# Kernel optimization log

Hardware: AMD Instinct MI355X
Metric: run time of the kernel (lower is better)

## Reference

```python
import jax, jax.numpy as jnp
import numpy as np

N = 50000          # nodes
E = 800000         # directed edges (before self loops)
H = 2              # attention heads
NEG_SLOPE = 0.2    # PyG GATv2 default
EPS = 1e-5         # GraphNorm eps
DIMS = [(3, 64), (64, 64), (64, 64)]


def _gatv2_layer(x, Wl, Wr, att, b, src, dst):
    # x: [N, din]; Wl, Wr: [din, H*C]; att: [H, C]; b: [C]
    n = x.shape[0]
    h, c = att.shape
    xl = (x @ Wl).reshape(n, h, c)   # source-side transform
    xr = (x @ Wr).reshape(n, h, c)   # target-side transform
    # edge-wise GATv2 score: a . leaky_relu(xl[j] + xr[i])
    e = jax.nn.leaky_relu(xl[src] + xr[dst], NEG_SLOPE)      # [E, H, C]
    logit = jnp.einsum('ehc,hc->eh', e, att)                 # [E, H]
    # segment softmax over incoming edges of each target node
    m = jax.ops.segment_max(logit, dst, num_segments=n)      # [N, H]
    a = jnp.exp(logit - m[dst])
    z = jax.ops.segment_sum(a, dst, num_segments=n)
    alpha = a / z[dst]                                       # [E, H]
    out = jax.ops.segment_sum(alpha[:, :, None] * xl[src], dst, num_segments=n)  # [N, H, C]
    return out.mean(axis=1) + b                              # concat=False -> head mean


def _graph_norm(x, w, b, ms):
    # single-graph GraphNorm: x -> w * (x - ms*mean) / sqrt(var + eps) + b
    mu = x.mean(axis=0)
    o = x - ms * mu
    var = (o * o).mean(axis=0)
    return w * o * jax.lax.rsqrt(var + EPS) + b


def setup_inputs() -> dict:
    key = jax.random.key(0)
    ks = jax.random.split(key, 2 + 3 * len(DIMS))
    inp = {
        'x': jax.random.normal(ks[0], (N, 3), dtype=jnp.float32),
        'edge_index': jax.random.randint(ks[1], (2, E), 0, N, dtype=jnp.int32),
    }
    for i, (din, dout) in enumerate(DIMS, start=1):
        k0, k1, k2 = ks[2 + 3 * (i - 1):2 + 3 * i]
        s_in = np.float32(1.0 / np.sqrt(din))
        s_att = np.float32(1.0 / np.sqrt(dout))
        inp[f'Wl{i}'] = jax.random.normal(k0, (din, H * dout), dtype=jnp.float32) * s_in
        inp[f'Wr{i}'] = jax.random.normal(k1, (din, H * dout), dtype=jnp.float32) * s_in
        inp[f'att{i}'] = jax.random.normal(k2, (H, dout), dtype=jnp.float32) * s_att
        inp[f'b{i}'] = jnp.zeros((dout,), dtype=jnp.float32)
        inp[f'gw{i}'] = jnp.ones((dout,), dtype=jnp.float32)
        inp[f'gb{i}'] = jnp.zeros((dout,), dtype=jnp.float32)
        inp[f'gm{i}'] = jnp.ones((dout,), dtype=jnp.float32)
    return inp


def reference(x, edge_index,
              Wl1, Wr1, att1, b1, gw1, gb1, gm1,
              Wl2, Wr2, att2, b2, gw2, gb2, gm2,
              Wl3, Wr3, att3, b3, gw3, gb3, gm3):
    n = x.shape[0]
    loop = jnp.arange(n, dtype=edge_index.dtype)
    src = jnp.concatenate([edge_index[0], loop])  # add_self_loops=True
    dst = jnp.concatenate([edge_index[1], loop])
    layers = [(Wl1, Wr1, att1, b1, gw1, gb1, gm1),
              (Wl2, Wr2, att2, b2, gw2, gb2, gm2),
              (Wl3, Wr3, att3, b3, gw3, gb3, gm3)]
    for Wl, Wr, att, b, gw, gb, gm in layers:
        x = _gatv2_layer(x, Wl, Wr, att, b, src, dst)
        x = jax.nn.relu(_graph_norm(x, gw, gb, gm))
    return x
```

## Files before the change

### kernel.cpp

```cpp
#include <hip/hip_runtime.h>
#include <math.h>

#define NN 50000
#define NE 800000
#define TE (NE + NN)
#define HC 128
#define NEG_SLOPE 0.2f
#define EPSV 1e-5f
#define NBUCK 64
#define GGRID 782
#define WTB 128
#define ZB 52
#define ZERO_N4 18644

typedef __attribute__((ext_vector_type(8))) short bf16x8;
typedef __attribute__((ext_vector_type(4))) float f32x4;
union BfU { uint4 u; bf16x8 b; };

__device__ __forceinline__ unsigned short f2bf(float x) {
    unsigned u = __float_as_uint(x);
    unsigned r = (u + 0x7fff + ((u >> 16) & 1)) >> 16;
    return (unsigned short)r;
}


__global__ __launch_bounds__(256) void count_k(const int* __restrict__ dst,
                                               int* __restrict__ cnt,
                                               int* __restrict__ rank) {
    int e = blockIdx.x * 256 + threadIdx.x;
    if (e >= TE) return;
    int d = (e < NE) ? dst[e] : (e - NE);
    rank[e] = atomicAdd(&cnt[d], 1);
}

__global__ __launch_bounds__(1024) void scan1_k(const int* __restrict__ cnt,
                                                int* __restrict__ excl,
                                                int* __restrict__ aux) {
    __shared__ int wsum[16];
    int tid = threadIdx.x;
    int gid = blockIdx.x * 1024 + tid;
    int lane = tid & 63, wid = tid >> 6;
    int v = (gid < NN) ? cnt[gid] : 0;
    int x = v;
#pragma unroll
    for (int off = 1; off < 64; off <<= 1) {
        int t = __shfl_up(x, off, 64);
        if (lane >= off) x += t;
    }
    if (lane == 63) wsum[wid] = x;
    __syncthreads();
    if (wid == 0 && lane < 16) {
        int y = wsum[lane];
#pragma unroll
        for (int off = 1; off < 16; off <<= 1) {
            int t = __shfl_up(y, off, 64);
            if (lane >= off) y += t;
        }
        wsum[lane] = y;
    }
    __syncthreads();
    int base = (wid > 0) ? wsum[wid - 1] : 0;
    int incl = base + x;
    if (gid < NN) excl[gid] = incl - v;
    if (tid == 1023) aux[blockIdx.x] = incl;
}

__global__ __launch_bounds__(256) void scatter_k(const int* __restrict__ srcp,
                                                 const int* __restrict__ dstp,
                                                 const int* __restrict__ excl,
                                                 const int* __restrict__ aux,
                                                 const int* __restrict__ rank,
                                                 int* __restrict__ row_ptr,
                                                 int* __restrict__ col,
                                                 int nblk) {
    __shared__ int auxs[64];
    if (threadIdx.x < 64) {
        int lane = threadIdx.x;
        int v = (lane < nblk) ? aux[lane] : 0;
        int x = v;
#pragma unroll
        for (int off = 1; off < 64; off <<= 1) {
            int t = __shfl_up(x, off, 64);
            if (lane >= off) x += t;
        }
        auxs[lane] = x - v;
    }
    __syncthreads();
    int e = blockIdx.x * 256 + threadIdx.x;
    if (e >= TE) return;
    if (e <= NN) row_ptr[e] = (e == NN) ? TE : excl[e] + auxs[e >> 10];
    int s, d;
    if (e < NE) { s = srcp[e]; d = dstp[e]; } else { s = e - NE; d = s; }
    col[excl[d] + auxs[d >> 10] + rank[e]] = s << 8;
}

__device__ __forceinline__ void store_xlp(char* xlp, int row, int c0, const float* a) {
    unsigned hsel = (unsigned)c0 >> 6;
    unsigned dd = (unsigned)c0 & 31;
    unsigned sub = (c0 & 32) ? 2u : 0u;
    char* q = xlp + (size_t)row * 256 + hsel * 128 + 4 * dd + sub;
#pragma unroll
    for (int j = 0; j < 4; ++j)
        *(unsigned short*)(q + 4 * j) = f2bf(a[j]);
}


__global__ __launch_bounds__(256) void init_k(const float* __restrict__ x,
                                              const float* __restrict__ Wl1,
                                              const float* __restrict__ Wr1,
                                              char* __restrict__ xlp,
                                              float* __restrict__ xr,
                                              const float* __restrict__ Wl2,
                                              const float* __restrict__ Wr2,
                                              const float* __restrict__ Wl3,
                                              const float* __restrict__ Wr3,
                                              unsigned short* __restrict__ wt2,
                                              unsigned short* __restrict__ wt3,
                                              float4* __restrict__ zero4) {
    __shared__ float xs[32][72];
    __shared__ float ws[32][260];
    int b = blockIdx.x;
    int tid = threadIdx.x;

    if (b >= GGRID) {
        if (b < GGRID + WTB) {
            int idx = (b - GGRID) * 256 + tid;
            int l = idx >> 14;
            int rem = idx & 16383;
            int k = rem >> 8;
            int c = rem & 255;
            const float* W = (l == 0) ? (c < 128 ? Wl2 : Wr2) : (c < 128 ? Wl3 : Wr3);
            float v = W[k * 128 + (c & 127)];
            unsigned short* wt = (l == 0) ? wt2 : wt3;
            wt[c * 64 + k] = f2bf(v);
        } else {
            float4 zv; zv.x = zv.y = zv.z = zv.w = 0.f;
            for (int i = (b - GGRID - WTB) * 256 + tid; i < ZERO_N4; i += ZB * 256)
                zero4[i] = zv;
        }
        return;
    }

    int row0 = b * 64;
    int row_t = (tid >> 5) * 8;
    int c0 = (tid & 31) * 4;
    const int K = 3;

    float acc0[8][4];
    float acc1[8][4];
#pragma unroll
    for (int i = 0; i < 8; ++i)
#pragma unroll
        for (int j = 0; j < 4; ++j) { acc0[i][j] = 0.f; acc1[i][j] = 0.f; }

    for (int i = tid; i < 64 * K; i += 256) {
        int r = i / K;
        int k = i - r * K;
        int row = row0 + r;
        xs[k][r] = (row < NN) ? x[(size_t)row * K + k] : 0.f;
    }
    for (int i = tid; i < K * 64; i += 256) {
        int k = i >> 6;
        int cq = i & 63;
        const float* srcp = (cq < 32) ? &Wl1[(size_t)k * 128 + cq * 4]
                                      : &Wr1[(size_t)k * 128 + (cq - 32) * 4];
        float4 v = *(const float4*)srcp;
        *(float4*)&ws[k][cq * 4] = v;
    }
    __syncthreads();
    for (int k = 0; k < K; ++k) {
        float4 a0 = *(float4*)&xs[k][row_t];
        float4 a1 = *(float4*)&xs[k][row_t + 4];
        float4 b0 = *(float4*)&ws[k][c0];
        float4 b1 = *(float4*)&ws[k][c0 + 128];
        float av[8] = {a0.x, a0.y, a0.z, a0.w, a1.x, a1.y, a1.z, a1.w};
        float bl[4] = {b0.x, b0.y, b0.z, b0.w};
        float br[4] = {b1.x, b1.y, b1.z, b1.w};
#pragma unroll
        for (int i = 0; i < 8; ++i)
#pragma unroll
            for (int j = 0; j < 4; ++j) {
                acc0[i][j] += av[i] * bl[j];
                acc1[i][j] += av[i] * br[j];
            }
    }
#pragma unroll
    for (int i = 0; i < 8; ++i) {
        int row = row0 + row_t + i;
        if (row < NN) {
            store_xlp(xlp, row, c0, acc0[i]);
            float4 o1; o1.x = acc1[i][0]; o1.y = acc1[i][1]; o1.z = acc1[i][2]; o1.w = acc1[i][3];
            *(float4*)&xr[(size_t)row * HC + c0] = o1;
        }
    }
}

__device__ __forceinline__ void reduce_stats(const float* __restrict__ stats,
                                             const float* __restrict__ gw,
                                             const float* __restrict__ gb,
                                             const float* __restrict__ gm,
                                             float (*part)[128],
                                             float* __restrict__ cf_out) {
    int tid = threadIdx.x;
    int w = tid >> 6;
    int lane = tid & 63;
    float s = 0.f, s2 = 0.f;
    for (int b = 16 * w; b < 16 * w + 16; ++b) {
        s += stats[b * 128 + lane];
        s2 += stats[b * 128 + 64 + lane];
    }
    part[w][lane] = s;
    part[w][64 + lane] = s2;
    __syncthreads();
    if (tid < 64) {
        int c = tid;
        float sum = (part[0][c] + part[1][c]) + (part[2][c] + part[3][c]);
        float sum2 = (part[0][64 + c] + part[1][64 + c]) + (part[2][64 + c] + part[3][64 + c]);
        float inv_n = 1.f / (float)NN;
        float mu = sum * inv_n;
        float ex2 = sum2 * inv_n;
        float g = gm[c];
        float var = ex2 - 2.f * g * mu * mu + g * g * mu * mu;
        float rs = rsqrtf(var + EPSV);
        cf_out[c] = gw[c] * rs;
        cf_out[64 + c] = gb[c] - gw[c] * rs * g * mu;
    }
    __syncthreads();
}


__global__ __launch_bounds__(256) void gemm_mfma(const unsigned* __restrict__ hbf,
                                                 const float* __restrict__ stats,
                                                 const float* __restrict__ gw,
                                                 const float* __restrict__ gb,
                                                 const float* __restrict__ gm,
                                                 const unsigned short* __restrict__ wt,
                                                 char* __restrict__ xlp,
                                                 float* __restrict__ xr,
                                                 int n) {
    __shared__ unsigned short xs[64][72];
    __shared__ float part[4][128];
    __shared__ float cfS[128];
    int tid = threadIdx.x;
    int row0 = blockIdx.x * 64;

    reduce_stats(stats, gw, gb, gm, part, cfS);

    {
        int r = tid >> 2;
        int q = tid & 3;
        int row = row0 + r;
        unsigned pk[8];
        if (row < n) {
            const unsigned* hp = hbf + (size_t)row * 32 + (q & 1) * 16;
            uint4 u0 = *(const uint4*)(hp + 0);
            uint4 u1 = *(const uint4*)(hp + 4);
            uint4 u2 = *(const uint4*)(hp + 8);
            uint4 u3 = *(const uint4*)(hp + 12);
            unsigned hv[16] = {u0.x, u0.y, u0.z, u0.w, u1.x, u1.y, u1.z, u1.w,
                               u2.x, u2.y, u2.z, u2.w, u3.x, u3.y, u3.z, u3.w};
            bool hi = (q >> 1) != 0;
#pragma unroll
            for (int i = 0; i < 4; ++i) {
                float4 v;
                v.x = hi ? __uint_as_float(hv[4 * i + 0] & 0xffff0000u) : __uint_as_float(hv[4 * i + 0] << 16);
                v.y = hi ? __uint_as_float(hv[4 * i + 1] & 0xffff0000u) : __uint_as_float(hv[4 * i + 1] << 16);
                v.z = hi ? __uint_as_float(hv[4 * i + 2] & 0xffff0000u) : __uint_as_float(hv[4 * i + 2] << 16);
                v.w = hi ? __uint_as_float(hv[4 * i + 3] & 0xffff0000u) : __uint_as_float(hv[4 * i + 3] << 16);
                float4 cw = *(const float4*)&cfS[q * 16 + 4 * i];
                float4 cb = *(const float4*)&cfS[64 + q * 16 + 4 * i];
                float r0 = fmaxf(fmaf(cw.x, v.x, cb.x), 0.f);
                float r1 = fmaxf(fmaf(cw.y, v.y, cb.y), 0.f);
                float r2 = fmaxf(fmaf(cw.z, v.z, cb.z), 0.f);
                float r3 = fmaxf(fmaf(cw.w, v.w, cb.w), 0.f);
                pk[2 * i]     = (unsigned)f2bf(r0) | ((unsigned)f2bf(r1) << 16);
                pk[2 * i + 1] = (unsigned)f2bf(r2) | ((unsigned)f2bf(r3) << 16);
            }
        } else {
#pragma unroll
            for (int i = 0; i < 8; ++i) pk[i] = 0;
        }
        uint4* dst = (uint4*)&xs[r][q * 16];
        dst[0] = make_uint4(pk[0], pk[1], pk[2], pk[3]);
        dst[1] = make_uint4(pk[4], pk[5], pk[6], pk[7]);
    }
    __syncthreads();

    int w = tid >> 6;
    int lane = tid & 63;
    int m = lane & 15;
    int quad = lane >> 4;

    BfU a0, a1;
    a0.u = *(const uint4*)&xs[16 * w + m][quad * 8];
    a1.u = *(const uint4*)&xs[16 * w + m][32 + quad * 8];

    const char* wtb = (const char*)wt + (size_t)(m * 128 + quad * 16);

    f32x4 acc[16];
#pragma unroll
    for (int c = 0; c < 16; ++c) acc[c] = (f32x4){0.f, 0.f, 0.f, 0.f};
#pragma unroll
    for (int c = 0; c < 16; ++c) {
        BfU b0, b1;
        b0.u = *(const uint4*)(wtb + c * 2048);
        b1.u = *(const uint4*)(wtb + c * 2048 + 64);
        acc[c] = __builtin_amdgcn_mfma_f32_16x16x32_bf16(a0.b, b0.b, acc[c], 0, 0, 0);
        acc[c] = __builtin_amdgcn_mfma_f32_16x16x32_bf16(a1.b, b1.b, acc[c], 0, 0, 0);
    }

    int rbase = row0 + 16 * w + quad * 4;
#pragma unroll
    for (int c = 8; c < 16; ++c) {
        int colx = 16 * (c - 8) + m;
#pragma unroll
        for (int r = 0; r < 4; ++r) {
            int row = rbase + r;
            if (row < n) xr[(size_t)row * 128 + colx] = acc[c][r];
        }
    }
#pragma unroll
    for (int pi = 0; pi < 4; ++pi) {
        int c = (pi & 1) + (pi >> 1) * 4;
        int head = pi >> 1;
        int dd = (pi & 1) * 16 + m;
#pragma unroll
        for (int r = 0; r < 4; ++r) {
            int row = rbase + r;
            if (row < n) {
                unsigned val = (unsigned)f2bf(acc[c][r]) | ((unsigned)f2bf(acc[c + 2][r]) << 16);
                *(unsigned*)(xlp + (size_t)row * 256 + head * 128 + 4 * dd) = val;
            }
        }
    }
}


__global__ __launch_bounds__(256) void coef_k(const float* __restrict__ stats,
                                              const float* __restrict__ gw,
                                              const float* __restrict__ gb,
                                              const float* __restrict__ gm,
                                              float* __restrict__ cf) {
    __shared__ float part[4][128];
    reduce_stats(stats, gw, gb, gm, part, cf);
}


__device__ __forceinline__ void attn_batch(const char* __restrict__ xlp, int lp4,
                                           const int* offs, float2 xrv,
                                           float2 c1, float2 c2,
                                           bool b16, int my, int rem,
                                           float& zacc, float2& o) {
    unsigned pk[8];
#pragma unroll
    for (int j = 0; j < 8; ++j)
        pk[j] = *(const unsigned*)(xlp + (unsigned)(offs[j] + lp4));
    float2 l[8];
#pragma unroll
    for (int j = 0; j < 8; ++j) {
        l[j].x = __uint_as_float(pk[j] << 16);
        l[j].y = __uint_as_float(pk[j] & 0xffff0000u);
    }
    float u[8];
#pragma unroll
    for (int j = 0; j < 8; ++j) {
        float2 t; t.x = l[j].x + xrv.x; t.y = l[j].y + xrv.y;
        float2 q;
        q.x = fmaf(c1.x, t.x, c2.x * fabsf(t.x));
        q.y = fmaf(c1.y, t.y, c2.y * fabsf(t.y));
        u[j] = q.x + q.y;
    }
#pragma unroll
    for (int j = 0; j < 8; ++j) u[j] += __shfl_xor(u[j], 16, 64);
    float w0 = b16 ? u[0] : u[1];
    float w1 = b16 ? u[2] : u[3];
    float w2 = b16 ? u[4] : u[5];
    float w3 = b16 ? u[6] : u[7];
#pragma unroll
    for (int off = 8; off > 0; off >>= 1) {
        w0 += __shfl_xor(w0, off, 64);
        w1 += __shfl_xor(w1, off, 64);
        w2 += __shfl_xor(w2, off, 64);
        w3 += __shfl_xor(w3, off, 64);
    }
    float e0 = __expf(w0);
    float e1 = __expf(w1);
    float e2 = __expf(w2);
    float e3 = __expf(w3);
    if (rem < 8) {
        if (my >= rem)     e0 = 0.f;
        if (2 + my >= rem) e1 = 0.f;
        if (4 + my >= rem) e2 = 0.f;
        if (6 + my >= rem) e3 = 0.f;
    }
    zacc += (e0 + e1) + (e2 + e3);
    float s0 = __shfl_xor(e0, 16, 64);
    float s1 = __shfl_xor(e1, 16, 64);
    float s2 = __shfl_xor(e2, 16, 64);
    float s3 = __shfl_xor(e3, 16, 64);
    float p0 = b16 ? e0 : s0;
    float p1 = b16 ? s0 : e0;
    float p2 = b16 ? e1 : s1;
    float p3 = b16 ? s1 : e1;
    float p4 = b16 ? e2 : s2;
    float p5 = b16 ? s2 : e2;
    float p6 = b16 ? e3 : s3;
    float p7 = b16 ? s3 : e3;
    o.x = fmaf(p0, l[0].x, o.x); o.y = fmaf(p0, l[0].y, o.y);
    o.x = fmaf(p1, l[1].x, o.x); o.y = fmaf(p1, l[1].y, o.y);
    o.x = fmaf(p2, l[2].x, o.x); o.y = fmaf(p2, l[2].y, o.y);
    o.x = fmaf(p3, l[3].x, o.x); o.y = fmaf(p3, l[3].y, o.y);
    o.x = fmaf(p4, l[4].x, o.x); o.y = fmaf(p4, l[4].y, o.y);
    o.x = fmaf(p5, l[5].x, o.x); o.y = fmaf(p5, l[5].y, o.y);
    o.x = fmaf(p6, l[6].x, o.x); o.y = fmaf(p6, l[6].y, o.y);
    o.x = fmaf(p7, l[7].x, o.x); o.y = fmaf(p7, l[7].y, o.y);
}

__global__ __launch_bounds__(256) void attn_k(const char* __restrict__ xlp,
                                              const float* __restrict__ xr,
                                              const float* __restrict__ att,
                                              const float* __restrict__ bias,
                                              const int* __restrict__ row_ptr,
                                              const int* __restrict__ coloff,
                                              unsigned* __restrict__ hout,
                                              float* __restrict__ stats) {
    __shared__ float sb[4][64];
    int tid = threadIdx.x;
    int lane = tid & 63;
    int w = tid >> 6;
    int node = blockIdx.x * 4 + w;
    int laneh = lane & 31;
    int lanebase = ((lane >> 5) << 8) | (laneh << 2);
    bool b16 = (lane & 16) == 0;
    int my = b16 ? 0 : 1;
    int lp4 = lane * 4;

    const char* xrc = (const char*)xr;
    unsigned nodeoff = (unsigned)node << 9;

    float2 xrv;
    xrv.x = *(const float*)(xrc + nodeoff + lanebase);
    xrv.y = *(const float*)(xrc + nodeoff + lanebase + 128);
    float a1 = att[lanebase >> 2];
    float a2 = att[(lanebase >> 2) + 32];
    float2 c1; c1.x = 0.6f * a1; c1.y = 0.6f * a2;
    float2 c2; c2.x = 0.4f * a1; c2.y = 0.4f * a2;

    float zacc = 0.f;
    float2 o; o.x = 0.f; o.y = 0.f;

    int beg = __builtin_amdgcn_readfirstlane(row_ptr[node]);
    int end = __builtin_amdgcn_readfirstlane(row_ptr[node + 1]);

    int idx = beg;
    for (; idx + 8 <= end; idx += 8) {
        int offs[8];
#pragma unroll
        for (int j = 0; j < 8; ++j) offs[j] = coloff[idx + j];
        attn_batch(xlp, lp4, offs, xrv, c1, c2, b16, my, 8, zacc, o);
    }
    if (idx < end) {
        int rem = end - idx;
        int end1 = end - 1;
        int offs[8];
#pragma unroll
        for (int j = 0; j < 8; ++j) offs[j] = coloff[min(idx + j, end1)];
        attn_batch(xlp, lp4, offs, xrv, c1, c2, b16, my, rem, zacc, o);
    }
    float z = zacc + __shfl_xor(zacc, 16, 64);
    float zi = 1.0f / z;
    float2 t; t.x = o.x * zi; t.y = o.y * zi;
    float u1 = __shfl_xor(t.x, 32, 64);
    float u2 = __shfl_xor(t.y, 32, 64);
    if (lane < 32) {
        float r1 = fmaf(0.5f, t.x + u1, bias[laneh]);
        float r2 = fmaf(0.5f, t.y + u2, bias[laneh + 32]);
        hout[(size_t)node * 32 + laneh] = (unsigned)f2bf(r1) | ((unsigned)f2bf(r2) << 16);
        sb[w][laneh] = r1;
        sb[w][laneh + 32] = r2;
    }
    __syncthreads();
    if (tid < 64) {
        int c = tid;
        float v0 = sb[0][c], v1 = sb[1][c], v2 = sb[2][c], v3 = sb[3][c];
        float s = (v0 + v1) + (v2 + v3);
        float s2 = fmaf(v0, v0, v1 * v1) + fmaf(v2, v2, v3 * v3);
        float* bkt = stats + (size_t)(blockIdx.x & (NBUCK - 1)) * 128;
        atomicAdd(&bkt[c], s);
        atomicAdd(&bkt[64 + c], s2);
    }
}


__global__ __launch_bounds__(256) void apply_k(const unsigned* __restrict__ h,
                                               const float* __restrict__ cf,
                                               float* __restrict__ y) {
    int i = blockIdx.x * 256 + threadIdx.x;
    if (i >= NN * 8) return;
    int node = i >> 3;
    int j = (i & 7) * 4;
    uint4 u = *(const uint4*)(h + (size_t)node * 32 + j);
    float4 lo, hi;
    lo.x = __uint_as_float(u.x << 16); hi.x = __uint_as_float(u.x & 0xffff0000u);
    lo.y = __uint_as_float(u.y << 16); hi.y = __uint_as_float(u.y & 0xffff0000u);
    lo.z = __uint_as_float(u.z << 16); hi.z = __uint_as_float(u.z & 0xffff0000u);
    lo.w = __uint_as_float(u.w << 16); hi.w = __uint_as_float(u.w & 0xffff0000u);
    float4 cwl = *(const float4*)&cf[j];
    float4 cbl = *(const float4*)&cf[64 + j];
    float4 cwh = *(const float4*)&cf[32 + j];
    float4 cbh = *(const float4*)&cf[96 + j];
    float4 rl, rh;
    rl.x = fmaxf(fmaf(cwl.x, lo.x, cbl.x), 0.f);
    rl.y = fmaxf(fmaf(cwl.y, lo.y, cbl.y), 0.f);
    rl.z = fmaxf(fmaf(cwl.z, lo.z, cbl.z), 0.f);
    rl.w = fmaxf(fmaf(cwl.w, lo.w, cbl.w), 0.f);
    rh.x = fmaxf(fmaf(cwh.x, hi.x, cbh.x), 0.f);
    rh.y = fmaxf(fmaf(cwh.y, hi.y, cbh.y), 0.f);
    rh.z = fmaxf(fmaf(cwh.z, hi.z, cbh.z), 0.f);
    rh.w = fmaxf(fmaf(cwh.w, hi.w, cbh.w), 0.f);
    *(float4*)&y[(size_t)node * 64 + j] = rl;
    *(float4*)&y[(size_t)node * 64 + 32 + j] = rh;
}


extern "C" void kernel_launch(void* const* d_in, const int* in_sizes, int n_in,
                              void* d_out, int out_size, void* d_ws, size_t ws_size,
                              hipStream_t stream) {
    const float* x0 = (const float*)d_in[0];
    const int* ei = (const int*)d_in[1];
    const int* srcp = ei;
    const int* dstp = ei + NE;

    const float* Wl[3], *Wr[3], *att[3], *bv[3], *gw[3], *gb[3], *gm[3];
    for (int l = 0; l < 3; ++l) {
        int base = 2 + 7 * l;
        Wl[l] = (const float*)d_in[base + 0];
        Wr[l] = (const float*)d_in[base + 1];
        att[l] = (const float*)d_in[base + 2];
        bv[l] = (const float*)d_in[base + 3];
        gw[l] = (const float*)d_in[base + 4];
        gb[l] = (const float*)d_in[base + 5];
        gm[l] = (const float*)d_in[base + 6];
    }

    char* p = (char*)d_ws;
    auto take = [&](size_t bytes) -> void* {
        void* r = (void*)p;
        p += (bytes + 255) & ~(size_t)255;
        return r;
    };
    char* xlp = (char*)take((size_t)NN * 256);
    float* xr = (float*)take((size_t)NN * 128 * 4);
    unsigned* hb = (unsigned*)take((size_t)NN * 32 * 4);
    char* zr = (char*)take(298304);
    float* stats = (float*)zr;
    int* cnt = (int*)(zr + 98304);
    int* excl = (int*)take((size_t)NN * 4);
    int* row_ptr = (int*)take((size_t)(NN + 1) * 4);
    int* rank = (int*)take((size_t)TE * 4);
    int* col = (int*)take((size_t)TE * 4);
    int* aux = (int*)take(64 * 4);
    float* cf3 = (float*)take(128 * 4);
    unsigned short* wt2 = (unsigned short*)take(16384 * 2);
    unsigned short* wt3 = (unsigned short*)take(16384 * 2);

    int nblk = (NN + 1023) / 1024;
    int egrid = (TE + 255) / 256;

    init_k<<<GGRID + WTB + ZB, 256, 0, stream>>>(x0, Wl[0], Wr[0], xlp, xr,
                                                 Wl[1], Wr[1], Wl[2], Wr[2],
                                                 wt2, wt3, (float4*)zr);
    count_k<<<egrid, 256, 0, stream>>>(dstp, cnt, rank);
    scan1_k<<<nblk, 1024, 0, stream>>>(cnt, excl, aux);
    scatter_k<<<egrid, 256, 0, stream>>>(srcp, dstp, excl, aux, rank, row_ptr, col, nblk);

    int ggrid = (NN + 63) / 64;
    int agrid = NN / 4;
    for (int l = 0; l < 3; ++l) {
        if (l > 0)
            gemm_mfma<<<ggrid, 256, 0, stream>>>(hb, stats + (size_t)(l - 1) * NBUCK * 128,
                                                 gw[l - 1], gb[l - 1], gm[l - 1],
                                                 (l == 1) ? wt2 : wt3, xlp, xr, NN);
        attn_k<<<agrid, 256, 0, stream>>>(xlp, xr, att[l], bv[l], row_ptr, col, hb,
                                          stats + (size_t)l * NBUCK * 128);
    }
    coef_k<<<1, 256, 0, stream>>>(stats + (size_t)2 * NBUCK * 128, gw[2], gb[2], gm[2], cf3);
    apply_k<<<(NN * 8 + 255) / 256, 256, 0, stream>>>(hb, cf3, (float*)d_out);
}
```

Measured before the change: 360.1 us.

## Software-pipeline neighbor gathers in attention and vectorize CSR build kernels

```diff
diff --git a/kernel.cpp b/kernel.cpp
--- a/kernel.cpp
+++ b/kernel.cpp
@@ -27,10 +27,20 @@
 __global__ __launch_bounds__(256) void count_k(const int* __restrict__ dst,
                                                int* __restrict__ cnt,
                                                int* __restrict__ rank) {
-    int e = blockIdx.x * 256 + threadIdx.x;
-    if (e >= TE) return;
-    int d = (e < NE) ? dst[e] : (e - NE);
-    rank[e] = atomicAdd(&cnt[d], 1);
+    int t = blockIdx.x * 256 + threadIdx.x;
+    if (t >= TE / 4) return;
+    int4 d4;
+    if (t < NE / 4) d4 = ((const int4*)dst)[t];
+    else {
+        int e = 4 * t - NE;
+        d4.x = e; d4.y = e + 1; d4.z = e + 2; d4.w = e + 3;
+    }
+    int4 r4;
+    r4.x = atomicAdd(&cnt[d4.x], 1);
+    r4.y = atomicAdd(&cnt[d4.y], 1);
+    r4.z = atomicAdd(&cnt[d4.z], 1);
+    r4.w = atomicAdd(&cnt[d4.w], 1);
+    ((int4*)rank)[t] = r4;
 }
 
 __global__ __launch_bounds__(1024) void scan1_k(const int* __restrict__ cnt,
@@ -86,12 +96,29 @@
         auxs[lane] = x - v;
     }
     __syncthreads();
-    int e = blockIdx.x * 256 + threadIdx.x;
-    if (e >= TE) return;
-    if (e <= NN) row_ptr[e] = (e == NN) ? TE : excl[e] + auxs[e >> 10];
-    int s, d;
-    if (e < NE) { s = srcp[e]; d = dstp[e]; } else { s = e - NE; d = s; }
-    col[excl[d] + auxs[d >> 10] + rank[e]] = s << 8;
+    int t = blockIdx.x * 256 + threadIdx.x;
+    if (t >= TE / 4) return;
+    int4 s4, d4;
+    if (t < NE / 4) {
+        s4 = ((const int4*)srcp)[t];
+        d4 = ((const int4*)dstp)[t];
+    } else {
+        int e = 4 * t - NE;
+        s4.x = e; s4.y = e + 1; s4.z = e + 2; s4.w = e + 3;
+        d4 = s4;
+    }
+    int4 r4 = ((const int4*)rank)[t];
+    col[excl[d4.x] + auxs[d4.x >> 10] + r4.x] = s4.x << 8;
+    col[excl[d4.y] + auxs[d4.y >> 10] + r4.y] = s4.y << 8;
+    col[excl[d4.z] + auxs[d4.z >> 10] + r4.z] = s4.z << 8;
+    col[excl[d4.w] + auxs[d4.w >> 10] + r4.w] = s4.w << 8;
+    if (t <= NN / 4) {
+#pragma unroll
+        for (int j = 0; j < 4; ++j) {
+            int i = 4 * t + j;
+            if (i <= NN) row_ptr[i] = (i == NN) ? TE : excl[i] + auxs[i >> 10];
+        }
+    }
 }
 
 __device__ __forceinline__ void store_xlp(char* xlp, int row, int c0, const float* a) {
@@ -346,15 +373,10 @@
 }
 
 
-__device__ __forceinline__ void attn_batch(const char* __restrict__ xlp, int lp4,
-                                           const int* offs, float2 xrv,
-                                           float2 c1, float2 c2,
-                                           bool b16, int my, int rem,
-                                           float& zacc, float2& o) {
-    unsigned pk[8];
-#pragma unroll
-    for (int j = 0; j < 8; ++j)
-        pk[j] = *(const unsigned*)(xlp + (unsigned)(offs[j] + lp4));
+__device__ __forceinline__ void attn_compute(const unsigned* pk, float2 xrv,
+                                             float2 c1, float2 c2,
+                                             bool b16, int my, int rem,
+                                             float& zacc, float2& o) {
     float2 l[8];
 #pragma unroll
     for (int j = 0; j < 8; ++j) {
@@ -451,21 +473,35 @@
 
     int beg = __builtin_amdgcn_readfirstlane(row_ptr[node]);
     int end = __builtin_amdgcn_readfirstlane(row_ptr[node + 1]);
-
+    int end1 = end - 1;
+    int nb = (end - beg + 7) >> 3;
+
+    unsigned pkc[8];
+    {
+#pragma unroll
+        for (int j = 0; j < 8; ++j) {
+            int off = coloff[min(beg + j, end1)];
+            pkc[j] = *(const unsigned*)(xlp + (unsigned)(off + lp4));
+        }
+    }
     int idx = beg;
-    for (; idx + 8 <= end; idx += 8) {
-        int offs[8];
-#pragma unroll
-        for (int j = 0; j < 8; ++j) offs[j] = coloff[idx + j];
-        attn_batch(xlp, lp4, offs, xrv, c1, c2, b16, my, 8, zacc, o);
-    }
-    if (idx < end) {
+    for (int b = 0; b < nb; ++b) {
+        unsigned pkn[8];
+        bool more = (b + 1 < nb);
+        if (more) {
+#pragma unroll
+            for (int j = 0; j < 8; ++j) {
+                int off = coloff[min(idx + 8 + j, end1)];
+                pkn[j] = *(const unsigned*)(xlp + (unsigned)(off + lp4));
+            }
+        }
         int rem = end - idx;
-        int end1 = end - 1;
-        int offs[8];
-#pragma unroll
-        for (int j = 0; j < 8; ++j) offs[j] = coloff[min(idx + j, end1)];
-        attn_batch(xlp, lp4, offs, xrv, c1, c2, b16, my, rem, zacc, o);
+        attn_compute(pkc, xrv, c1, c2, b16, my, rem, zacc, o);
+        if (more) {
+#pragma unroll
+            for (int j = 0; j < 8; ++j) pkc[j] = pkn[j];
+        }
+        idx += 8;
     }
     float z = zacc + __shfl_xor(zacc, 16, 64);
     float zi = 1.0f / z;
@@ -565,14 +601,14 @@
     unsigned short* wt3 = (unsigned short*)take(16384 * 2);
 
     int nblk = (NN + 1023) / 1024;
-    int egrid = (TE + 255) / 256;
+    int egrid4 = (TE / 4 + 255) / 256;
 
     init_k<<<GGRID + WTB + ZB, 256, 0, stream>>>(x0, Wl[0], Wr[0], xlp, xr,
                                                  Wl[1], Wr[1], Wl[2], Wr[2],
                                                  wt2, wt3, (float4*)zr);
-    count_k<<<egrid, 256, 0, stream>>>(dstp, cnt, rank);
+    count_k<<<egrid4, 256, 0, stream>>>(dstp, cnt, rank);
     scan1_k<<<nblk, 1024, 0, stream>>>(cnt, excl, aux);
-    scatter_k<<<egrid, 256, 0, stream>>>(srcp, dstp, excl, aux, rank, row_ptr, col, nblk);
+    scatter_k<<<egrid4, 256, 0, stream>>>(srcp, dstp, excl, aux, rank, row_ptr, col, nblk);
 
     int ggrid = (NN + 63) / 64;
     int agrid = NN / 4;
```

Result: slower. 367.4 us (+2.0%).

## Remap attention wave to four edges per iteration with 16-byte gathers

Applied to the files above, without the earlier changes.

```diff
diff --git a/kernel.cpp b/kernel.cpp
--- a/kernel.cpp
+++ b/kernel.cpp
@@ -346,76 +346,6 @@
 }
 
 
-__device__ __forceinline__ void attn_batch(const char* __restrict__ xlp, int lp4,
-                                           const int* offs, float2 xrv,
-                                           float2 c1, float2 c2,
-                                           bool b16, int my, int rem,
-                                           float& zacc, float2& o) {
-    unsigned pk[8];
-#pragma unroll
-    for (int j = 0; j < 8; ++j)
-        pk[j] = *(const unsigned*)(xlp + (unsigned)(offs[j] + lp4));
-    float2 l[8];
-#pragma unroll
-    for (int j = 0; j < 8; ++j) {
-        l[j].x = __uint_as_float(pk[j] << 16);
-        l[j].y = __uint_as_float(pk[j] & 0xffff0000u);
-    }
-    float u[8];
-#pragma unroll
-    for (int j = 0; j < 8; ++j) {
-        float2 t; t.x = l[j].x + xrv.x; t.y = l[j].y + xrv.y;
-        float2 q;
-        q.x = fmaf(c1.x, t.x, c2.x * fabsf(t.x));
-        q.y = fmaf(c1.y, t.y, c2.y * fabsf(t.y));
-        u[j] = q.x + q.y;
-    }
-#pragma unroll
-    for (int j = 0; j < 8; ++j) u[j] += __shfl_xor(u[j], 16, 64);
-    float w0 = b16 ? u[0] : u[1];
-    float w1 = b16 ? u[2] : u[3];
-    float w2 = b16 ? u[4] : u[5];
-    float w3 = b16 ? u[6] : u[7];
-#pragma unroll
-    for (int off = 8; off > 0; off >>= 1) {
-        w0 += __shfl_xor(w0, off, 64);
-        w1 += __shfl_xor(w1, off, 64);
-        w2 += __shfl_xor(w2, off, 64);
-        w3 += __shfl_xor(w3, off, 64);
-    }
-    float e0 = __expf(w0);
-    float e1 = __expf(w1);
-    float e2 = __expf(w2);
-    float e3 = __expf(w3);
-    if (rem < 8) {
-        if (my >= rem)     e0 = 0.f;
-        if (2 + my >= rem) e1 = 0.f;
-        if (4 + my >= rem) e2 = 0.f;
-        if (6 + my >= rem) e3 = 0.f;
-    }
-    zacc += (e0 + e1) + (e2 + e3);
-    float s0 = __shfl_xor(e0, 16, 64);
-    float s1 = __shfl_xor(e1, 16, 64);
-    float s2 = __shfl_xor(e2, 16, 64);
-    float s3 = __shfl_xor(e3, 16, 64);
-    float p0 = b16 ? e0 : s0;
-    float p1 = b16 ? s0 : e0;
-    float p2 = b16 ? e1 : s1;
-    float p3 = b16 ? s1 : e1;
-    float p4 = b16 ? e2 : s2;
-    float p5 = b16 ? s2 : e2;
-    float p6 = b16 ? e3 : s3;
-    float p7 = b16 ? s3 : e3;
-    o.x = fmaf(p0, l[0].x, o.x); o.y = fmaf(p0, l[0].y, o.y);
-    o.x = fmaf(p1, l[1].x, o.x); o.y = fmaf(p1, l[1].y, o.y);
-    o.x = fmaf(p2, l[2].x, o.x); o.y = fmaf(p2, l[2].y, o.y);
-    o.x = fmaf(p3, l[3].x, o.x); o.y = fmaf(p3, l[3].y, o.y);
-    o.x = fmaf(p4, l[4].x, o.x); o.y = fmaf(p4, l[4].y, o.y);
-    o.x = fmaf(p5, l[5].x, o.x); o.y = fmaf(p5, l[5].y, o.y);
-    o.x = fmaf(p6, l[6].x, o.x); o.y = fmaf(p6, l[6].y, o.y);
-    o.x = fmaf(p7, l[7].x, o.x); o.y = fmaf(p7, l[7].y, o.y);
-}
-
 __global__ __launch_bounds__(256) void attn_k(const char* __restrict__ xlp,
                                               const float* __restrict__ xr,
                                               const float* __restrict__ att,
@@ -429,55 +359,115 @@
     int lane = tid & 63;
     int w = tid >> 6;
     int node = blockIdx.x * 4 + w;
-    int laneh = lane & 31;
-    int lanebase = ((lane >> 5) << 8) | (laneh << 2);
-    bool b16 = (lane & 16) == 0;
-    int my = b16 ? 0 : 1;
-    int lp4 = lane * 4;
-
-    const char* xrc = (const char*)xr;
-    unsigned nodeoff = (unsigned)node << 9;
-
-    float2 xrv;
-    xrv.x = *(const float*)(xrc + nodeoff + lanebase);
-    xrv.y = *(const float*)(xrc + nodeoff + lanebase + 128);
-    float a1 = att[lanebase >> 2];
-    float a2 = att[(lanebase >> 2) + 32];
-    float2 c1; c1.x = 0.6f * a1; c1.y = 0.6f * a2;
-    float2 c2; c2.x = 0.4f * a1; c2.y = 0.4f * a2;
+    int g = lane >> 4;
+    int li = lane & 15;
+    int h = li >> 3;
+    int m = li & 7;
+    int li16 = li * 16;
+
+    const float* xrow = xr + (size_t)node * 128 + h * 64 + 4 * m;
+    float4 xlo = *(const float4*)xrow;
+    float4 xhi = *(const float4*)(xrow + 32);
+    const float* arow = att + h * 64 + 4 * m;
+    float4 alo = *(const float4*)arow;
+    float4 ahi = *(const float4*)(arow + 32);
+    float4 c1lo, c2lo, c1hi, c2hi;
+    c1lo.x = 0.6f * alo.x; c1lo.y = 0.6f * alo.y; c1lo.z = 0.6f * alo.z; c1lo.w = 0.6f * alo.w;
+    c2lo.x = 0.4f * alo.x; c2lo.y = 0.4f * alo.y; c2lo.z = 0.4f * alo.z; c2lo.w = 0.4f * alo.w;
+    c1hi.x = 0.6f * ahi.x; c1hi.y = 0.6f * ahi.y; c1hi.z = 0.6f * ahi.z; c1hi.w = 0.6f * ahi.w;
+    c2hi.x = 0.4f * ahi.x; c2hi.y = 0.4f * ahi.y; c2hi.z = 0.4f * ahi.z; c2hi.w = 0.4f * ahi.w;
 
     float zacc = 0.f;
-    float2 o; o.x = 0.f; o.y = 0.f;
+    float4 olo; olo.x = olo.y = olo.z = olo.w = 0.f;
+    float4 ohi; ohi.x = ohi.y = ohi.z = ohi.w = 0.f;
 
     int beg = __builtin_amdgcn_readfirstlane(row_ptr[node]);
     int end = __builtin_amdgcn_readfirstlane(row_ptr[node + 1]);
-
-    int idx = beg;
-    for (; idx + 8 <= end; idx += 8) {
-        int offs[8];
-#pragma unroll
-        for (int j = 0; j < 8; ++j) offs[j] = coloff[idx + j];
-        attn_batch(xlp, lp4, offs, xrv, c1, c2, b16, my, 8, zacc, o);
-    }
-    if (idx < end) {
-        int rem = end - idx;
-        int end1 = end - 1;
-        int offs[8];
-#pragma unroll
-        for (int j = 0; j < 8; ++j) offs[j] = coloff[min(idx + j, end1)];
-        attn_batch(xlp, lp4, offs, xrv, c1, c2, b16, my, rem, zacc, o);
-    }
-    float z = zacc + __shfl_xor(zacc, 16, 64);
-    float zi = 1.0f / z;
-    float2 t; t.x = o.x * zi; t.y = o.y * zi;
-    float u1 = __shfl_xor(t.x, 32, 64);
-    float u2 = __shfl_xor(t.y, 32, 64);
-    if (lane < 32) {
-        float r1 = fmaf(0.5f, t.x + u1, bias[laneh]);
-        float r2 = fmaf(0.5f, t.y + u2, bias[laneh + 32]);
-        hout[(size_t)node * 32 + laneh] = (unsigned)f2bf(r1) | ((unsigned)f2bf(r2) << 16);
-        sb[w][laneh] = r1;
-        sb[w][laneh + 32] = r2;
+    int end1 = end - 1;
+
+    for (int idx = beg; idx < end; idx += 4) {
+        int o0 = coloff[idx];
+        int o1 = coloff[min(idx + 1, end1)];
+        int o2 = coloff[min(idx + 2, end1)];
+        int o3 = coloff[min(idx + 3, end1)];
+        int off = (g == 0) ? o0 : (g == 1) ? o1 : (g == 2) ? o2 : o3;
+        uint4 pk = *(const uint4*)(xlp + (unsigned)(off + li16));
+        float llo0 = __uint_as_float(pk.x << 16), lhi0 = __uint_as_float(pk.x & 0xffff0000u);
+        float llo1 = __uint_as_float(pk.y << 16), lhi1 = __uint_as_float(pk.y & 0xffff0000u);
+        float llo2 = __uint_as_float(pk.z << 16), lhi2 = __uint_as_float(pk.z & 0xffff0000u);
+        float llo3 = __uint_as_float(pk.w << 16), lhi3 = __uint_as_float(pk.w & 0xffff0000u);
+        float t0 = llo0 + xlo.x;
+        float t1 = llo1 + xlo.y;
+        float t2 = llo2 + xlo.z;
+        float t3 = llo3 + xlo.w;
+        float t4 = lhi0 + xhi.x;
+        float t5 = lhi1 + xhi.y;
+        float t6 = lhi2 + xhi.z;
+        float t7 = lhi3 + xhi.w;
+        float u = fmaf(c1lo.x, t0, c2lo.x * fabsf(t0));
+        u += fmaf(c1lo.y, t1, c2lo.y * fabsf(t1));
+        u += fmaf(c1lo.z, t2, c2lo.z * fabsf(t2));
+        u += fmaf(c1lo.w, t3, c2lo.w * fabsf(t3));
+        u += fmaf(c1hi.x, t4, c2hi.x * fabsf(t4));
+        u += fmaf(c1hi.y, t5, c2hi.y * fabsf(t5));
+        u += fmaf(c1hi.z, t6, c2hi.z * fabsf(t6));
+        u += fmaf(c1hi.w, t7, c2hi.w * fabsf(t7));
+        u += __shfl_xor(u, 1, 64);
+        u += __shfl_xor(u, 2, 64);
+        u += __shfl_xor(u, 4, 64);
+        float e = __expf(u);
+        if (idx + g >= end) e = 0.f;
+        zacc += e;
+        olo.x = fmaf(e, llo0, olo.x);
+        olo.y = fmaf(e, llo1, olo.y);
+        olo.z = fmaf(e, llo2, olo.z);
+        olo.w = fmaf(e, llo3, olo.w);
+        ohi.x = fmaf(e, lhi0, ohi.x);
+        ohi.y = fmaf(e, lhi1, ohi.y);
+        ohi.z = fmaf(e, lhi2, ohi.z);
+        ohi.w = fmaf(e, lhi3, ohi.w);
+    }
+    zacc += __shfl_xor(zacc, 16, 64);
+    zacc += __shfl_xor(zacc, 32, 64);
+    olo.x += __shfl_xor(olo.x, 16, 64); olo.x += __shfl_xor(olo.x, 32, 64);
+    olo.y += __shfl_xor(olo.y, 16, 64); olo.y += __shfl_xor(olo.y, 32, 64);
+    olo.z += __shfl_xor(olo.z, 16, 64); olo.z += __shfl_xor(olo.z, 32, 64);
+    olo.w += __shfl_xor(olo.w, 16, 64); olo.w += __shfl_xor(olo.w, 32, 64);
+    ohi.x += __shfl_xor(ohi.x, 16, 64); ohi.x += __shfl_xor(ohi.x, 32, 64);
+    ohi.y += __shfl_xor(ohi.y, 16, 64); ohi.y += __shfl_xor(ohi.y, 32, 64);
+    ohi.z += __shfl_xor(ohi.z, 16, 64); ohi.z += __shfl_xor(ohi.z, 32, 64);
+    ohi.w += __shfl_xor(ohi.w, 16, 64); ohi.w += __shfl_xor(ohi.w, 32, 64);
+    float zi = 1.0f / zacc;
+    float tl0 = olo.x * zi, tl1 = olo.y * zi, tl2 = olo.z * zi, tl3 = olo.w * zi;
+    float th0 = ohi.x * zi, th1 = ohi.y * zi, th2 = ohi.z * zi, th3 = ohi.w * zi;
+    float rl0 = 0.5f * (tl0 + __shfl_xor(tl0, 8, 64));
+    float rl1 = 0.5f * (tl1 + __shfl_xor(tl1, 8, 64));
+    float rl2 = 0.5f * (tl2 + __shfl_xor(tl2, 8, 64));
+    float rl3 = 0.5f * (tl3 + __shfl_xor(tl3, 8, 64));
+    float rh0 = 0.5f * (th0 + __shfl_xor(th0, 8, 64));
+    float rh1 = 0.5f * (th1 + __shfl_xor(th1, 8, 64));
+    float rh2 = 0.5f * (th2 + __shfl_xor(th2, 8, 64));
+    float rh3 = 0.5f * (th3 + __shfl_xor(th3, 8, 64));
+    const float* brow = bias + 4 * m;
+    float4 blo = *(const float4*)brow;
+    float4 bhi = *(const float4*)(brow + 32);
+    rl0 += blo.x; rl1 += blo.y; rl2 += blo.z; rl3 += blo.w;
+    rh0 += bhi.x; rh1 += bhi.y; rh2 += bhi.z; rh3 += bhi.w;
+    if (g == 0 && li < 8) {
+        uint4 pko;
+        pko.x = (unsigned)f2bf(rl0) | ((unsigned)f2bf(rh0) << 16);
+        pko.y = (unsigned)f2bf(rl1) | ((unsigned)f2bf(rh1) << 16);
+        pko.z = (unsigned)f2bf(rl2) | ((unsigned)f2bf(rh2) << 16);
+        pko.w = (unsigned)f2bf(rl3) | ((unsigned)f2bf(rh3) << 16);
+        *(uint4*)(hout + (size_t)node * 32 + 4 * m) = pko;
+        sb[w][4 * m + 0] = rl0;
+        sb[w][4 * m + 1] = rl1;
+        sb[w][4 * m + 2] = rl2;
+        sb[w][4 * m + 3] = rl3;
+        sb[w][4 * m + 32] = rh0;
+        sb[w][4 * m + 33] = rh1;
+        sb[w][4 * m + 34] = rh2;
+        sb[w][4 * m + 35] = rh3;
     }
     __syncthreads();
     if (tid < 64) {
```

New measurement: 362.7 us. About the same (+0.7%).
